# Performance work log

Measured on AMD Instinct MI355X. Metric: run time of the kernel, lower is better.

Reference implementation:

```python
import jax, jax.numpy as jnp
from jax import lax
import numpy as np
from functools import partial

B, N, T, H, L = 16, 256, 4, 128, 2
VOCAB, OUT_VOCAB, MAX_STEPS = 1000, 1000, 15


def setup_inputs() -> dict:
    key = jax.random.key(0)
    ks = jax.random.split(key, 13)
    data = jax.random.randint(ks[0], (B, N, T), 0, VOCAB)
    true_branch_nodes = jax.random.randint(ks[1], (B, N), 0, N)
    false_branch_nodes = jax.random.randint(ks[2], (B, N), 0, N)
    exit_index = jax.random.randint(ks[3], (B,), 0, N)
    steps = jax.random.randint(ks[4], (B,), 1, MAX_STEPS + 1)
    s_in = 1.0 / np.sqrt(H)
    s_cat = 1.0 / np.sqrt(2 * L * H)
    embed = jax.random.uniform(ks[5], (VOCAB, H), jnp.float32, -0.1, 0.1)
    Wi = jax.random.normal(ks[6], (L, H, 4 * H), jnp.float32) * s_in
    Wh = jax.random.normal(ks[7], (L, H, 4 * H), jnp.float32) * s_in
    b_lstm = jnp.zeros((L, 4 * H), jnp.float32)
    Wb = jax.random.normal(ks[8], (2 * L * H, 2), jnp.float32) * s_cat
    bb = jax.random.normal(ks[9], (2,), jnp.float32) * 1e-6
    Wo = jax.random.normal(ks[10], (2 * L * H, OUT_VOCAB), jnp.float32) * s_cat
    bo = jax.random.normal(ks[11], (OUT_VOCAB,), jnp.float32) * 1e-6
    return dict(data=data, true_branch_nodes=true_branch_nodes,
                false_branch_nodes=false_branch_nodes, exit_index=exit_index,
                steps=steps, embed=embed, Wi=Wi, Wh=Wh, b_lstm=b_lstm,
                Wb=Wb, bb=bb, Wo=Wo, bo=bo)


def _lstm_step(Wi_l, Wh_l, b_l, c, h, x):
    # flax LSTMCell math: gates from input (no bias) + recurrent (bias)
    z = x @ Wi_l + h @ Wh_l + b_l  # [..., 4H]
    i, f, g, o = jnp.split(z, 4, axis=-1)
    c2 = jax.nn.sigmoid(f) * c + jax.nn.sigmoid(i) * jnp.tanh(g)
    h2 = jax.nn.sigmoid(o) * jnp.tanh(c2)
    return c2, h2


def _forward(data, true_branch_nodes, false_branch_nodes, exit_index, steps,
             embed, Wi, Wh, b_lstm, Wb, bb, Wo, bo):
    emb = embed[data]                       # [B, N, T, H]
    cs = jnp.zeros((L, B, N, H), embed.dtype)
    hs = jnp.zeros((L, B, N, H), embed.dtype)
    ip = jnp.zeros((B, N), embed.dtype).at[:, 0].set(1.0)
    b_idx = jnp.arange(B)

    seg_b = jax.vmap(partial(jax.ops.segment_sum, num_segments=N))        # [B,N,...] , [B,N]
    seg_lb = jax.vmap(seg_b, in_axes=(0, None))                           # [L,B,N,H]

    def execute(cs, hs):
        # run the stacked LSTM over the T statement tokens at every node
        def tok_step(carry, x_t):
            cs, hs = carry
            inp = x_t
            nc, nh = [], []
            for l in range(L):
                c2, h2 = _lstm_step(Wi[l], Wh[l], b_lstm[l], cs[l], hs[l], inp)
                nc.append(c2); nh.append(h2)
                inp = h2
            return (jnp.stack(nc), jnp.stack(nh)), None
        (cs, hs), _ = lax.scan(tok_step, (cs, hs), jnp.moveaxis(emb, 2, 0))
        return cs, hs

    def step(carry, _):
        cs, hs, ip, idx = carry
        cs_c, hs_c = execute(cs, hs)
        # exit node keeps its previous hidden state
        cs_c = cs_c.at[:, b_idx, exit_index].set(cs[:, b_idx, exit_index])
        hs_c = hs_c.at[:, b_idx, exit_index].set(hs[:, b_idx, exit_index])
        # branch decision from concatenated (c, h) of every layer: [B, N, 2LH]
        feats = jnp.concatenate([x for l in range(L) for x in (cs_c[l], hs_c[l])], axis=-1)
        branch = jax.nn.softmax(feats @ Wb + bb, axis=-1)
        wt = branch[..., 0] * ip            # [B, N]
        wf = branch[..., 1] * ip
        ip_new = seg_b(wt, true_branch_nodes) + seg_b(wf, false_branch_nodes)
        denom = (ip_new + 1e-7)[None, :, :, None]
        def agg(h):
            return (seg_lb(h * wt[None, :, :, None], true_branch_nodes)
                    + seg_lb(h * wf[None, :, :, None], false_branch_nodes)) / denom
        cs_new, hs_new = agg(cs_c), agg(hs_c)
        live = idx < steps                   # [B]
        cs = jnp.where(live[None, :, None, None], cs_new, cs)
        hs = jnp.where(live[None, :, None, None], hs_new, hs)
        ip = jnp.where(live[:, None], ip_new, ip)
        return (cs, hs, ip, idx + 1), None

    (cs, hs, ip, _), _ = lax.scan(step, (cs, hs, ip, jnp.zeros((), jnp.int32)),
                                  None, length=MAX_STEPS)
    fc = cs[:, b_idx, exit_index]           # [L, B, H]
    fh = hs[:, b_idx, exit_index]
    final = jnp.concatenate([x for l in range(L) for x in (fc[l], fh[l])], axis=-1)
    logits = final @ Wo + bo                # [B, OUT_VOCAB]
    return logits[:, None, :]


def reference(data, true_branch_nodes, false_branch_nodes, exit_index, steps,
              embed, Wi, Wh, b_lstm, Wb, bb, Wo, bo):
    return _forward(data, true_branch_nodes, false_branch_nodes, exit_index,
                    steps, embed, Wi, Wh, b_lstm, Wb, bb, Wo, bo)
```

## Files before the change

### kernel.cpp

```cpp
#include <hip/hip_runtime.h>
#include <hip/hip_bf16.h>
#include <stdint.h>
#include <stddef.h>

static constexpr int BB = 16, NN = 256, TT = 4, HH = 128;
static constexpr int MM = BB * NN;
static constexpr int CC = 512;
static constexpr int OUTV = 1000;
static constexpr int MAXS = 15;
static constexpr int SP = 132;

typedef float f32x4 __attribute__((ext_vector_type(4)));
typedef short s16x8 __attribute__((ext_vector_type(8)));

__device__ __forceinline__ float sigf(float x) { return 1.0f / (1.0f + __expf(-x)); }
__device__ __forceinline__ float tanhr(float x) { return 2.0f / (1.0f + __expf(-2.0f * x)) - 1.0f; }
__device__ __forceinline__ unsigned short f2bu(float a) {
  return __builtin_bit_cast(unsigned short, __float2bfloat16(a));
}
__device__ __forceinline__ unsigned int packh(float a, float b) {
  return (unsigned int)f2bu(a) | ((unsigned int)f2bu(b) << 16);
}
__device__ __forceinline__ float blo(unsigned int u) { return __builtin_bit_cast(float, u << 16); }
__device__ __forceinline__ float bhi(unsigned int u) { return __builtin_bit_cast(float, u & 0xffff0000u); }


__global__ void init_kernel(int* __restrict__ count) {
  int i = blockIdx.x * 256 + threadIdx.x;
  if (i < MM) count[i] = 0;
}

__global__ void swz_all_kernel(const float* __restrict__ Wh0, const float* __restrict__ Wi1,
                               const float* __restrict__ Wh1, unsigned short* __restrict__ swz) {
  int i = blockIdx.x * 256 + threadIdx.x;
  int mtx = i >> 16, ii = i & 65535;
  const float* W = (mtx == 0) ? Wh0 : (mtx == 1) ? Wi1 : Wh1;
  int j = ii & 7, ln = (ii >> 3) & 63, kb = (ii >> 9) & 3, ct = ii >> 11;
  int n = ln & 15, q = ln >> 4;
  swz[i] = f2bu(W[(kb * 32 + q * 8 + j) * CC + ct * 16 + n]);
}

__global__ void xw0tab_kernel(const float* __restrict__ embed, const float* __restrict__ Wi0,
                              const float* __restrict__ b0, float* __restrict__ tab) {
  const int v0 = blockIdx.x * 8;
  const int j = threadIdx.x;
  __shared__ float A[8][HH];
  for (int s = j; s < 8 * HH; s += 256) {
    int r = s >> 7, k = s & 127;
    int v = v0 + r; if (v >= OUTV) v = OUTV - 1;
    A[r][k] = embed[(size_t)v * HH + k];
  }
  __syncthreads();
  float za[8], zb[8];
  {
    float ba = b0[j], bbv = b0[j + 256];
#pragma unroll
    for (int r = 0; r < 8; ++r) { za[r] = ba; zb[r] = bbv; }
  }
#pragma unroll 4
  for (int k = 0; k < HH; ++k) {
    float wa = Wi0[k * CC + j], wb = Wi0[k * CC + j + 256];
#pragma unroll
    for (int r = 0; r < 8; ++r) { za[r] += A[r][k] * wa; zb[r] += A[r][k] * wb; }
  }
#pragma unroll
  for (int r = 0; r < 8; ++r) {
    tab[(size_t)(v0 + r) * CC + j] = za[r];
    tab[(size_t)(v0 + r) * CC + j + 256] = zb[r];
  }
}

__global__ void edge_count(const int* __restrict__ tb, const int* __restrict__ fb,
                           int* __restrict__ count) {
  int e = blockIdx.x * blockDim.x + threadIdx.x;
  if (e >= 2 * MM) return;
  int b = e >> 9, r = e & 511, n = r >> 1, bit = r & 1;
  int tgt = bit ? fb[b * NN + n] : tb[b * NN + n];
  atomicAdd(&count[b * NN + tgt], 1);
}

__global__ void edge_scan(int* __restrict__ count, int* __restrict__ offs) {
  int b = blockIdx.x, tid = threadIdx.x;
  __shared__ int s[256];
  int v = count[b * NN + tid];
  s[tid] = v;
  __syncthreads();
  for (int off = 1; off < 256; off <<= 1) {
    int t = (tid >= off) ? s[tid - off] : 0;
    __syncthreads();
    s[tid] += t;
    __syncthreads();
  }
  offs[b * NN + tid] = b * 2 * NN + s[tid] - v;
  count[b * NN + tid] = 0;
  if (b == 0 && tid == 0) offs[MM] = 2 * MM;
}

__global__ void edge_fill(const int* __restrict__ tb, const int* __restrict__ fb,
                          const int* __restrict__ offs, int* __restrict__ cursor,
                          int* __restrict__ edges) {
  int e = blockIdx.x * blockDim.x + threadIdx.x;
  if (e >= 2 * MM) return;
  int b = e >> 9, r = e & 511, n = r >> 1, bit = r & 1;
  int tgt = bit ? fb[b * NN + n] : tb[b * NN + n];
  int pos = offs[b * NN + tgt] + atomicAdd(&cursor[b * NN + tgt], 1);
  edges[pos] = (n << 1) | bit;
}


__global__ __launch_bounds__(512, 2) void step_kernel(
    float* __restrict__ Sc0g, float* __restrict__ Sh0g,
    float* __restrict__ Sc1g, float* __restrict__ Sh1g,
    const unsigned int* __restrict__ Pr, unsigned int* __restrict__ Pw,
    const float* __restrict__ wtR, const float* __restrict__ wfR,
    float* __restrict__ wtW, float* __restrict__ wfW,
    const int* __restrict__ offs, const int* __restrict__ edges,
    const float* __restrict__ tab,
    const unsigned short* __restrict__ swzWh0, const unsigned short* __restrict__ swzWi1,
    const unsigned short* __restrict__ swzWh1, const float* __restrict__ b1,
    const float* __restrict__ Wb, const float* __restrict__ bb,
    const int* __restrict__ data, const int* __restrict__ exi,
    const int* __restrict__ steps, int step) {
  const int B = blockIdx.x;
  const int b = (B & 7) | (((B >> 3) & 1) << 3);
  const int g16 = B >> 4;
  const int row0 = b * NN + g16 * 16;
  const int sb = steps[b];
  const bool aggLive = (step >= 1) && ((step - 1) < sb);
  const bool lstmLive = (step < sb);
  if (!aggLive && !lstmLive) return;

  const int tid = threadIdx.x;
  const int w = tid >> 6;
  const int lane = tid & 63;
  const int n16 = lane & 15, qq = lane >> 4;
  const int kcol = w * 16 + n16;
  const int basePos = ((kcol >> 5) * 64 + ((kcol >> 3) & 3) * 16) * 8 + (kcol & 7);

  __shared__ float c0L[16 * SP], h0L[16 * SP], c1L[16 * SP], h1L[16 * SP];
  __shared__ __align__(16) unsigned short hA0[2048], hA1[2048];
  __shared__ float exitP[512];
  __shared__ float ipL[16];
  __shared__ int toks[64];

  if (aggLive) {
    const int l = tid & 31;
    const int m = tid >> 5;
    const int node = row0 + m;
    const int beg = offs[node], end = offs[node + 1];
    float ac0[4] = {0,0,0,0}, ah0[4] = {0,0,0,0}, ac1[4] = {0,0,0,0}, ah1[4] = {0,0,0,0};
    float wsum = 0.f;
    for (int e = beg; e < end; ++e) {
      int rec = edges[e];
      int src = (b << 8) + (rec >> 1);
      float wv = (rec & 1) ? wfR[src] : wtR[src];
      wsum += wv;
      const uint4* pr = (const uint4*)(Pr + (size_t)src * 256 + 8 * l);
      uint4 u0 = pr[0], u1 = pr[1];
      ac0[0] += wv * blo(u0.x); ac0[1] += wv * bhi(u0.x);
      ac0[2] += wv * blo(u0.y); ac0[3] += wv * bhi(u0.y);
      ah0[0] += wv * blo(u0.z); ah0[1] += wv * bhi(u0.z);
      ah0[2] += wv * blo(u0.w); ah0[3] += wv * bhi(u0.w);
      ac1[0] += wv * blo(u1.x); ac1[1] += wv * bhi(u1.x);
      ac1[2] += wv * blo(u1.y); ac1[3] += wv * bhi(u1.y);
      ah1[0] += wv * blo(u1.z); ah1[1] += wv * bhi(u1.z);
      ah1[2] += wv * blo(u1.w); ah1[3] += wv * bhi(u1.w);
    }
    float inv = 1.0f / (wsum + 1e-7f);
    float4 o0 = { ac0[0]*inv, ac0[1]*inv, ac0[2]*inv, ac0[3]*inv };
    float4 o1 = { ah0[0]*inv, ah0[1]*inv, ah0[2]*inv, ah0[3]*inv };
    float4 o2 = { ac1[0]*inv, ac1[1]*inv, ac1[2]*inv, ac1[3]*inv };
    float4 o3 = { ah1[0]*inv, ah1[1]*inv, ah1[2]*inv, ah1[3]*inv };
    ((float4*)c0L)[m * (SP / 4) + l] = o0;
    ((float4*)h0L)[m * (SP / 4) + l] = o1;
    ((float4*)c1L)[m * (SP / 4) + l] = o2;
    ((float4*)h1L)[m * (SP / 4) + l] = o3;
    if (l == 0) ipL[m] = wsum;
    if (!lstmLive) {
      ((float4*)Sc0g)[node * 32 + l] = o0;
      ((float4*)Sh0g)[node * 32 + l] = o1;
      ((float4*)Sc1g)[node * 32 + l] = o2;
      ((float4*)Sh1g)[node * 32 + l] = o3;
    }
  } else {
    for (int i2 = tid; i2 < 16 * HH; i2 += 512) {
      int m = i2 >> 7, k = i2 & 127;
      c0L[m * SP + k] = 0.f; h0L[m * SP + k] = 0.f;
      c1L[m * SP + k] = 0.f; h1L[m * SP + k] = 0.f;
    }
    if (tid < 16) ipL[tid] = (((row0 + tid) & (NN - 1)) == 0) ? 1.0f : 0.0f;
  }
  if (!lstmLive) return;

  s16x8 B0f[4][4], B1f[4][4];
  const s16x8* pWh0 = (const s16x8*)swzWh0;
  const s16x8* pWh1 = (const s16x8*)swzWh1;
  const s16x8* pWi1 = (const s16x8*)swzWi1;
  float b1v[4];
#pragma unroll
  for (int g = 0; g < 4; ++g) {
    int ci = w + 8 * g;
#pragma unroll
    for (int kb = 0; kb < 4; ++kb) {
      B0f[g][kb] = pWh0[(ci * 4 + kb) * 64 + lane];
      B1f[g][kb] = pWh1[(ci * 4 + kb) * 64 + lane];
    }
    b1v[g] = b1[ci * 16 + n16];
  }

  const int exnode = exi[b];
  const int exm = exnode - (g16 * 16);
  if (tid < 64) toks[tid] = data[(row0 + (tid >> 2)) * TT + (tid & 3)];
  __syncthreads();

  if (exm >= 0 && exm < 16 && tid < 128) {
    exitP[tid] = c0L[exm * SP + tid];
    exitP[128 + tid] = h0L[exm * SP + tid];
    exitP[256 + tid] = c1L[exm * SP + tid];
    exitP[384 + tid] = h1L[exm * SP + tid];
  }

  float c0r[4], c1r[4], h0r[4], h1r[4];
#pragma unroll
  for (int r = 0; r < 4; ++r) {
    int m = qq * 4 + r;
    c0r[r] = c0L[m * SP + kcol];
    c1r[r] = c1L[m * SP + kcol];
    h0r[r] = h0L[m * SP + kcol];
    h1r[r] = h1L[m * SP + kcol];
    hA0[basePos + m * 8] = f2bu(h0r[r]);
    hA1[basePos + m * 8] = f2bu(h1r[r]);
  }
  __syncthreads();

  const s16x8* hA0v = (const s16x8*)hA0;
  const s16x8* hA1v = (const s16x8*)hA1;

  for (int t = 0; t < TT; ++t) {
    s16x8 a0[4], a1b[4];
#pragma unroll
    for (int kb = 0; kb < 4; ++kb) { a0[kb] = hA0v[kb * 64 + lane]; a1b[kb] = hA1v[kb * 64 + lane]; }
    f32x4 d0[4];
#pragma unroll
    for (int g = 0; g < 4; ++g) {
      int colz = (w + 8 * g) * 16 + n16;
#pragma unroll
      for (int r = 0; r < 4; ++r)
        d0[g][r] = tab[(size_t)toks[(qq * 4 + r) * 4 + t] * CC + colz];
    }
    __syncthreads();

#pragma unroll
    for (int g = 0; g < 4; ++g)
#pragma unroll
      for (int kb = 0; kb < 4; ++kb)
        d0[g] = __builtin_amdgcn_mfma_f32_16x16x32_bf16(a0[kb], B0f[g][kb], d0[g], 0, 0, 0);

#pragma unroll
    for (int r = 0; r < 4; ++r) {
      float cn = sigf(d0[1][r]) * c0r[r] + sigf(d0[0][r]) * tanhr(d0[2][r]);
      float hn = sigf(d0[3][r]) * tanhr(cn);
      c0r[r] = cn; h0r[r] = hn;
      hA0[basePos + (qq * 4 + r) * 8] = f2bu(hn);
    }
    __syncthreads();

    s16x8 a1a[4];
#pragma unroll
    for (int kb = 0; kb < 4; ++kb) a1a[kb] = hA0v[kb * 64 + lane];
    f32x4 d1[4];
#pragma unroll
    for (int g = 0; g < 4; ++g) {
      int ci = w + 8 * g;
      s16x8 wi[4];
#pragma unroll
      for (int kb = 0; kb < 4; ++kb) wi[kb] = pWi1[(ci * 4 + kb) * 64 + lane];
      f32x4 d = { b1v[g], b1v[g], b1v[g], b1v[g] };
#pragma unroll
      for (int kb = 0; kb < 4; ++kb)
        d = __builtin_amdgcn_mfma_f32_16x16x32_bf16(a1a[kb], wi[kb], d, 0, 0, 0);
#pragma unroll
      for (int kb = 0; kb < 4; ++kb)
        d = __builtin_amdgcn_mfma_f32_16x16x32_bf16(a1b[kb], B1f[g][kb], d, 0, 0, 0);
      d1[g] = d;
    }

#pragma unroll
    for (int r = 0; r < 4; ++r) {
      float cn = sigf(d1[1][r]) * c1r[r] + sigf(d1[0][r]) * tanhr(d1[2][r]);
      float hn = sigf(d1[3][r]) * tanhr(cn);
      c1r[r] = cn; h1r[r] = hn;
      hA1[basePos + (qq * 4 + r) * 8] = f2bu(hn);
    }
    __syncthreads();
  }

#pragma unroll
  for (int r = 0; r < 4; ++r) {
    int m = qq * 4 + r;
    c0L[m * SP + kcol] = c0r[r];
    h0L[m * SP + kcol] = h0r[r];
    c1L[m * SP + kcol] = c1r[r];
    h1L[m * SP + kcol] = h1r[r];
  }
  __syncthreads();

  {
    const int m = tid >> 5, sub = tid & 31;
    const int row = row0 + m;
    const bool isExit = (m == exm);
    float z0 = 0.f, z1 = 0.f;
#pragma unroll
    for (int u = 0; u < 16; ++u) {
      int k = u * 32 + sub;
      int seg = k >> 7, kk = k & 127;
      float fk;
      if (isExit) {
        fk = exitP[seg * 128 + kk];
      } else {
        fk = (seg == 0) ? c0L[m * SP + kk] : (seg == 1) ? h0L[m * SP + kk]
           : (seg == 2) ? c1L[m * SP + kk] : h1L[m * SP + kk];
      }
      z0 += fk * Wb[2 * k];
      z1 += fk * Wb[2 * k + 1];
    }
#pragma unroll
    for (int off = 16; off >= 1; off >>= 1) {
      z0 += __shfl_xor(z0, off);
      z1 += __shfl_xor(z1, off);
    }
    if (sub == 0) {
      z0 += bb[0]; z1 += bb[1];
      float mx = fmaxf(z0, z1);
      float e0 = __expf(z0 - mx), e1 = __expf(z1 - mx);
      float inv = 1.0f / (e0 + e1);
      float ipv = ipL[m];
      wtW[row] = e0 * inv * ipv;
      wfW[row] = e1 * inv * ipv;
    }
  }

  {
    const int m = tid >> 5, l = tid & 31;
    const bool ex = (m == exm);
    const int grow = row0 + m;
    float f0[4], f1[4], f2[4], f3[4];
#pragma unroll
    for (int i = 0; i < 4; ++i) {
      int k = 4 * l + i;
      f0[i] = ex ? exitP[k] : c0L[m * SP + k];
      f1[i] = ex ? exitP[128 + k] : h0L[m * SP + k];
      f2[i] = ex ? exitP[256 + k] : c1L[m * SP + k];
      f3[i] = ex ? exitP[384 + k] : h1L[m * SP + k];
    }
    uint4 o0 = { packh(f0[0], f0[1]), packh(f0[2], f0[3]),
                 packh(f1[0], f1[1]), packh(f1[2], f1[3]) };
    uint4 o1 = { packh(f2[0], f2[1]), packh(f2[2], f2[3]),
                 packh(f3[0], f3[1]), packh(f3[2], f3[3]) };
    uint4* pw = (uint4*)(Pw + (size_t)grow * 256 + 8 * l);
    pw[0] = o0; pw[1] = o1;
  }
}

__global__ void final_kernel(const float* __restrict__ Sc0, const float* __restrict__ Sh0,
                             const float* __restrict__ Sc1, const float* __restrict__ Sh1,
                             const int* __restrict__ exi, const float* __restrict__ Wo,
                             const float* __restrict__ bo, float* __restrict__ out) {
  const int b = blockIdx.x >> 2;
  const int vt = blockIdx.x & 3;
  const int tid = threadIdx.x;
  __shared__ float f[512];
  int row = b * NN + exi[b];
  if (tid < 128) {
    size_t g = (size_t)row * HH + tid;
    f[tid] = Sc0[g];
    f[128 + tid] = Sh0[g];
    f[256 + tid] = Sc1[g];
    f[384 + tid] = Sh1[g];
  }
  __syncthreads();
  if (tid < 250) {
    int v = vt * 250 + tid;
    float acc = bo[v];
#pragma unroll 8
    for (int k = 0; k < 512; ++k) acc += f[k] * Wo[(size_t)k * OUTV + v];
    out[b * OUTV + v] = acc;
  }
}

__global__ void zero_out_kernel(float* __restrict__ out, int n) {
  int i = blockIdx.x * blockDim.x + threadIdx.x;
  if (i < n) out[i] = 0.0f;
}


extern "C" void kernel_launch(void* const* d_in, const int* in_sizes, int n_in,
                              void* d_out, int out_size, void* d_ws, size_t ws_size,
                              hipStream_t stream) {
  const int* data = (const int*)d_in[0];
  const int* tb   = (const int*)d_in[1];
  const int* fb   = (const int*)d_in[2];
  const int* exi  = (const int*)d_in[3];
  const int* steps = (const int*)d_in[4];
  const float* embed = (const float*)d_in[5];
  const float* Wi = (const float*)d_in[6];
  const float* Wh = (const float*)d_in[7];
  const float* bl = (const float*)d_in[8];
  const float* Wb = (const float*)d_in[9];
  const float* bb = (const float*)d_in[10];
  const float* Wo = (const float*)d_in[11];
  const float* bo = (const float*)d_in[12];
  float* out = (float*)d_out;

  const float* Wi0 = Wi;
  const float* Wi1 = Wi + HH * CC;
  const float* Wh0 = Wh;
  const float* Wh1 = Wh + HH * CC;
  const float* b0 = bl;
  const float* b1 = bl + CC;

  float* ws = (float*)d_ws;
  size_t off = 0;
  float* tab = ws + off;  off += (size_t)1024 * CC;
  float* Sc0 = ws + off;  off += (size_t)MM * HH;
  float* Sh0 = ws + off;  off += (size_t)MM * HH;
  float* Sc1 = ws + off;  off += (size_t)MM * HH;
  float* Sh1 = ws + off;  off += (size_t)MM * HH;
  unsigned int* PA = (unsigned int*)(ws + off); off += (size_t)MM * 256;
  unsigned int* PB = (unsigned int*)(ws + off); off += (size_t)MM * 256;
  unsigned short* swz = (unsigned short*)(ws + off); off += 3 * 32768;
  float* wtA = ws + off;  off += MM;
  float* wfA = ws + off;  off += MM;
  float* wtB = ws + off;  off += MM;
  float* wfB = ws + off;  off += MM;
  int* count = (int*)(ws + off); off += MM;
  int* offs  = (int*)(ws + off); off += MM + 16;
  int* edges = (int*)(ws + off); off += 2 * MM;
  (void)in_sizes; (void)n_in; (void)out_size;

  if (ws_size < off * sizeof(float)) {
    zero_out_kernel<<<(BB * OUTV + 255) / 256, 256, 0, stream>>>(out, BB * OUTV);
    return;
  }

  unsigned short* swzWh0 = swz;
  unsigned short* swzWi1 = swz + 65536;
  unsigned short* swzWh1 = swz + 2 * 65536;

  init_kernel<<<16, 256, 0, stream>>>(count);
  swz_all_kernel<<<768, 256, 0, stream>>>(Wh0, Wi1, Wh1, swz);
  xw0tab_kernel<<<128, 256, 0, stream>>>(embed, Wi0, b0, tab);
  edge_count<<<32, 256, 0, stream>>>(tb, fb, count);
  edge_scan<<<BB, 256, 0, stream>>>(count, offs);
  edge_fill<<<32, 256, 0, stream>>>(tb, fb, offs, count, edges);

  for (int s = 0; s <= MAXS; ++s) {
    unsigned int* Pwp = (s & 1) ? PB : PA;
    const unsigned int* Prp = (s & 1) ? PA : PB;
    float* wtWp = (s & 1) ? wtB : wtA;
    float* wfWp = (s & 1) ? wfB : wfA;
    const float* wtRp = (s & 1) ? wtA : wtB;
    const float* wfRp = (s & 1) ? wfA : wfB;
    step_kernel<<<MM / 16, 512, 0, stream>>>(
        Sc0, Sh0, Sc1, Sh1, Prp, Pwp,
        wtRp, wfRp, wtWp, wfWp,
        offs, edges, tab, swzWh0, swzWi1, swzWh1, b1, Wb, bb,
        data, exi, steps, s);
  }
  final_kernel<<<BB * 4, 256, 0, stream>>>(Sc0, Sh0, Sc1, Sh1, exi, Wo, bo, out);
}
```

Before: 559.7 us.

## Fuse setup kernels, hoist weight loads, double-buffer LSTM hidden tiles

The four CSR-building kernels become a single per-batch csr_kernel that does its counting, scan and fill in shared memory. The weight-swizzle and embedding-table kernels merge into one prep_kernel, so six setup launches become two. In step_kernel, the register loads of the recurrent weight fragments and the token fetch move ahead of the aggregation phase so their latency can overlap it. The hA0/hA1 staging buffers are double-buffered, which removes one __syncthreads per timestep, and the min-blocks hint in launch_bounds is dropped, giving the compiler more register freedom at the possible cost of occupancy.

```diff
diff --git a/kernel.cpp b/kernel.cpp
--- a/kernel.cpp
+++ b/kernel.cpp
@@ -25,32 +25,57 @@
 __device__ __forceinline__ float bhi(unsigned int u) { return __builtin_bit_cast(float, u & 0xffff0000u); }
 
 
-__global__ void init_kernel(int* __restrict__ count) {
-  int i = blockIdx.x * 256 + threadIdx.x;
-  if (i < MM) count[i] = 0;
-}
-
-__global__ void swz_all_kernel(const float* __restrict__ Wh0, const float* __restrict__ Wi1,
-                               const float* __restrict__ Wh1, unsigned short* __restrict__ swz) {
-  int i = blockIdx.x * 256 + threadIdx.x;
-  int mtx = i >> 16, ii = i & 65535;
-  const float* W = (mtx == 0) ? Wh0 : (mtx == 1) ? Wi1 : Wh1;
-  int j = ii & 7, ln = (ii >> 3) & 63, kb = (ii >> 9) & 3, ct = ii >> 11;
-  int n = ln & 15, q = ln >> 4;
-  swz[i] = f2bu(W[(kb * 32 + q * 8 + j) * CC + ct * 16 + n]);
-}
-
-__global__ void xw0tab_kernel(const float* __restrict__ embed, const float* __restrict__ Wi0,
-                              const float* __restrict__ b0, float* __restrict__ tab) {
-  const int v0 = blockIdx.x * 8;
-  const int j = threadIdx.x;
+__global__ __launch_bounds__(512) void csr_kernel(const int* __restrict__ tb,
+                                                  const int* __restrict__ fb,
+                                                  int* __restrict__ offs,
+                                                  int* __restrict__ edges) {
+  const int blk = blockIdx.x;
+  const int tid = threadIdx.x;
+  __shared__ int cnt[256], sc[256], cur[256];
+  if (tid < 256) cnt[tid] = 0;
+  __syncthreads();
+  const int n = tid >> 1, bit = tid & 1;
+  const int tgt = bit ? fb[blk * NN + n] : tb[blk * NN + n];
+  atomicAdd(&cnt[tgt], 1);
+  __syncthreads();
+  if (tid < 256) sc[tid] = cnt[tid];
+  __syncthreads();
+  for (int ofs = 1; ofs < 256; ofs <<= 1) {
+    int t2 = (tid < 256 && tid >= ofs) ? sc[tid - ofs] : 0;
+    __syncthreads();
+    if (tid < 256) sc[tid] += t2;
+    __syncthreads();
+  }
+  if (tid < 256) { offs[blk * NN + tid] = blk * 2 * NN + sc[tid] - cnt[tid]; cur[tid] = 0; }
+  if (blk == 0 && tid == 0) offs[MM] = 2 * MM;
+  __syncthreads();
+  int lpos = sc[tgt] - cnt[tgt] + atomicAdd(&cur[tgt], 1);
+  edges[blk * 2 * NN + lpos] = (n << 1) | bit;
+}
+
+__global__ __launch_bounds__(256) void prep_kernel(
+    const float* __restrict__ Wh0, const float* __restrict__ Wi1, const float* __restrict__ Wh1,
+    const float* __restrict__ embed, const float* __restrict__ Wi0, const float* __restrict__ b0,
+    unsigned short* __restrict__ swz, float* __restrict__ tab) {
+  const int blk = blockIdx.x;
+  const int tid = threadIdx.x;
+  if (blk < 768) {
+    int i = blk * 256 + tid;
+    int mtx = i >> 16, ii = i & 65535;
+    const float* W = (mtx == 0) ? Wh0 : (mtx == 1) ? Wi1 : Wh1;
+    int j = ii & 7, ln = (ii >> 3) & 63, kb = (ii >> 9) & 3, ct = ii >> 11;
+    int n = ln & 15, q = ln >> 4;
+    swz[i] = f2bu(W[(kb * 32 + q * 8 + j) * CC + ct * 16 + n]);
+    return;
+  }
+  const int v0 = (blk - 768) * 8;
   __shared__ float A[8][HH];
-  for (int s = j; s < 8 * HH; s += 256) {
+  for (int s = tid; s < 8 * HH; s += 256) {
     int r = s >> 7, k = s & 127;
-    int v = v0 + r; if (v >= OUTV) v = OUTV - 1;
-    A[r][k] = embed[(size_t)v * HH + k];
-  }
-  __syncthreads();
+    A[r][k] = embed[(size_t)(v0 + r) * HH + k];
+  }
+  __syncthreads();
+  const int j = tid;
   float za[8], zb[8];
   {
     float ba = b0[j], bbv = b0[j + 256];
@@ -70,45 +95,8 @@
   }
 }
 
-__global__ void edge_count(const int* __restrict__ tb, const int* __restrict__ fb,
-                           int* __restrict__ count) {
-  int e = blockIdx.x * blockDim.x + threadIdx.x;
-  if (e >= 2 * MM) return;
-  int b = e >> 9, r = e & 511, n = r >> 1, bit = r & 1;
-  int tgt = bit ? fb[b * NN + n] : tb[b * NN + n];
-  atomicAdd(&count[b * NN + tgt], 1);
-}
-
-__global__ void edge_scan(int* __restrict__ count, int* __restrict__ offs) {
-  int b = blockIdx.x, tid = threadIdx.x;
-  __shared__ int s[256];
-  int v = count[b * NN + tid];
-  s[tid] = v;
-  __syncthreads();
-  for (int off = 1; off < 256; off <<= 1) {
-    int t = (tid >= off) ? s[tid - off] : 0;
-    __syncthreads();
-    s[tid] += t;
-    __syncthreads();
-  }
-  offs[b * NN + tid] = b * 2 * NN + s[tid] - v;
-  count[b * NN + tid] = 0;
-  if (b == 0 && tid == 0) offs[MM] = 2 * MM;
-}
-
-__global__ void edge_fill(const int* __restrict__ tb, const int* __restrict__ fb,
-                          const int* __restrict__ offs, int* __restrict__ cursor,
-                          int* __restrict__ edges) {
-  int e = blockIdx.x * blockDim.x + threadIdx.x;
-  if (e >= 2 * MM) return;
-  int b = e >> 9, r = e & 511, n = r >> 1, bit = r & 1;
-  int tgt = bit ? fb[b * NN + n] : tb[b * NN + n];
-  int pos = offs[b * NN + tgt] + atomicAdd(&cursor[b * NN + tgt], 1);
-  edges[pos] = (n << 1) | bit;
-}
-
-
-__global__ __launch_bounds__(512, 2) void step_kernel(
+
+__global__ __launch_bounds__(512) void step_kernel(
     float* __restrict__ Sc0g, float* __restrict__ Sh0g,
     float* __restrict__ Sc1g, float* __restrict__ Sh1g,
     const unsigned int* __restrict__ Pr, unsigned int* __restrict__ Pw,
@@ -138,10 +126,29 @@
   const int basePos = ((kcol >> 5) * 64 + ((kcol >> 3) & 3) * 16) * 8 + (kcol & 7);
 
   __shared__ float c0L[16 * SP], h0L[16 * SP], c1L[16 * SP], h1L[16 * SP];
-  __shared__ __align__(16) unsigned short hA0[2048], hA1[2048];
+  __shared__ __align__(16) unsigned short hA0[2][2048], hA1[2][2048];
   __shared__ float exitP[512];
   __shared__ float ipL[16];
   __shared__ int toks[64];
+
+  s16x8 B0f[4][4], B1f[4][4];
+  float b1v[4];
+  const s16x8* pWh0 = (const s16x8*)swzWh0;
+  const s16x8* pWh1 = (const s16x8*)swzWh1;
+  const s16x8* pWi1 = (const s16x8*)swzWi1;
+  if (lstmLive) {
+#pragma unroll
+    for (int g = 0; g < 4; ++g) {
+      int ci = w + 8 * g;
+#pragma unroll
+      for (int kb = 0; kb < 4; ++kb) {
+        B0f[g][kb] = pWh0[(ci * 4 + kb) * 64 + lane];
+        B1f[g][kb] = pWh1[(ci * 4 + kb) * 64 + lane];
+      }
+      b1v[g] = b1[ci * 16 + n16];
+    }
+    if (tid < 64) toks[tid] = data[(row0 + (tid >> 2)) * TT + (tid & 3)];
+  }
 
   if (aggLive) {
     const int l = tid & 31;
@@ -192,25 +199,8 @@
   }
   if (!lstmLive) return;
 
-  s16x8 B0f[4][4], B1f[4][4];
-  const s16x8* pWh0 = (const s16x8*)swzWh0;
-  const s16x8* pWh1 = (const s16x8*)swzWh1;
-  const s16x8* pWi1 = (const s16x8*)swzWi1;
-  float b1v[4];
-#pragma unroll
-  for (int g = 0; g < 4; ++g) {
-    int ci = w + 8 * g;
-#pragma unroll
-    for (int kb = 0; kb < 4; ++kb) {
-      B0f[g][kb] = pWh0[(ci * 4 + kb) * 64 + lane];
-      B1f[g][kb] = pWh1[(ci * 4 + kb) * 64 + lane];
-    }
-    b1v[g] = b1[ci * 16 + n16];
-  }
-
   const int exnode = exi[b];
   const int exm = exnode - (g16 * 16);
-  if (tid < 64) toks[tid] = data[(row0 + (tid >> 2)) * TT + (tid & 3)];
   __syncthreads();
 
   if (exm >= 0 && exm < 16 && tid < 128) {
@@ -228,18 +218,19 @@
     c1r[r] = c1L[m * SP + kcol];
     h0r[r] = h0L[m * SP + kcol];
     h1r[r] = h1L[m * SP + kcol];
-    hA0[basePos + m * 8] = f2bu(h0r[r]);
-    hA1[basePos + m * 8] = f2bu(h1r[r]);
-  }
-  __syncthreads();
-
-  const s16x8* hA0v = (const s16x8*)hA0;
-  const s16x8* hA1v = (const s16x8*)hA1;
-
+    hA0[0][basePos + m * 8] = f2bu(h0r[r]);
+    hA1[0][basePos + m * 8] = f2bu(h1r[r]);
+  }
+  __syncthreads();
+
+  int cur = 0;
   for (int t = 0; t < TT; ++t) {
+    const int nxt = cur ^ 1;
+    const s16x8* hA0c = (const s16x8*)hA0[cur];
+    const s16x8* hA1c = (const s16x8*)hA1[cur];
     s16x8 a0[4], a1b[4];
 #pragma unroll
-    for (int kb = 0; kb < 4; ++kb) { a0[kb] = hA0v[kb * 64 + lane]; a1b[kb] = hA1v[kb * 64 + lane]; }
+    for (int kb = 0; kb < 4; ++kb) { a0[kb] = hA0c[kb * 64 + lane]; a1b[kb] = hA1c[kb * 64 + lane]; }
     f32x4 d0[4];
 #pragma unroll
     for (int g = 0; g < 4; ++g) {
@@ -248,7 +239,6 @@
       for (int r = 0; r < 4; ++r)
         d0[g][r] = tab[(size_t)toks[(qq * 4 + r) * 4 + t] * CC + colz];
     }
-    __syncthreads();
 
 #pragma unroll
     for (int g = 0; g < 4; ++g)
@@ -261,13 +251,14 @@
       float cn = sigf(d0[1][r]) * c0r[r] + sigf(d0[0][r]) * tanhr(d0[2][r]);
       float hn = sigf(d0[3][r]) * tanhr(cn);
       c0r[r] = cn; h0r[r] = hn;
-      hA0[basePos + (qq * 4 + r) * 8] = f2bu(hn);
+      hA0[nxt][basePos + (qq * 4 + r) * 8] = f2bu(hn);
     }
     __syncthreads();
 
+    const s16x8* hA0n = (const s16x8*)hA0[nxt];
     s16x8 a1a[4];
 #pragma unroll
-    for (int kb = 0; kb < 4; ++kb) a1a[kb] = hA0v[kb * 64 + lane];
+    for (int kb = 0; kb < 4; ++kb) a1a[kb] = hA0n[kb * 64 + lane];
     f32x4 d1[4];
 #pragma unroll
     for (int g = 0; g < 4; ++g) {
@@ -290,9 +281,10 @@
       float cn = sigf(d1[1][r]) * c1r[r] + sigf(d1[0][r]) * tanhr(d1[2][r]);
       float hn = sigf(d1[3][r]) * tanhr(cn);
       c1r[r] = cn; h1r[r] = hn;
-      hA1[basePos + (qq * 4 + r) * 8] = f2bu(hn);
+      hA1[nxt][basePos + (qq * 4 + r) * 8] = f2bu(hn);
     }
     __syncthreads();
+    cur = nxt;
   }
 
 #pragma unroll
@@ -433,7 +425,6 @@
   float* wfA = ws + off;  off += MM;
   float* wtB = ws + off;  off += MM;
   float* wfB = ws + off;  off += MM;
-  int* count = (int*)(ws + off); off += MM;
   int* offs  = (int*)(ws + off); off += MM + 16;
   int* edges = (int*)(ws + off); off += 2 * MM;
   (void)in_sizes; (void)n_in; (void)out_size;
@@ -447,12 +438,8 @@
   unsigned short* swzWi1 = swz + 65536;
   unsigned short* swzWh1 = swz + 2 * 65536;
 
-  init_kernel<<<16, 256, 0, stream>>>(count);
-  swz_all_kernel<<<768, 256, 0, stream>>>(Wh0, Wi1, Wh1, swz);
-  xw0tab_kernel<<<128, 256, 0, stream>>>(embed, Wi0, b0, tab);
-  edge_count<<<32, 256, 0, stream>>>(tb, fb, count);
-  edge_scan<<<BB, 256, 0, stream>>>(count, offs);
-  edge_fill<<<32, 256, 0, stream>>>(tb, fb, offs, count, edges);
+  csr_kernel<<<BB, 512, 0, stream>>>(tb, fb, offs, edges);
+  prep_kernel<<<893, 256, 0, stream>>>(Wh0, Wi1, Wh1, embed, Wi0, b0, swz, tab);
 
   for (int s = 0; s <= MAXS; ++s) {
     unsigned int* Pwp = (s & 1) ? PB : PA;
```

Result: no change. 551.1 us (-1.5%).
